# Performance work log

Hardware: AMD Instinct MI355X
Metric: run time of the kernel (lower is better)

The kernel has to match this reference:

```python
import jax, jax.numpy as jnp
import numpy as np

B, T, F_IN, NF, K, H, NOUT = 512, 800, 3, 128, 15, 150, 10
EPS = 1e-5


def hard_sigmoid(x):
    # Keras-style hard sigmoid used by LSTMHardSigmoid gates
    return jnp.clip(0.2 * x + 0.5, 0.0, 1.0)


def adabn(x, gamma, beta, axes):
    # AdaBN: normalize with current-batch statistics, then learned affine.
    m = jnp.mean(x, axis=axes, keepdims=True)
    v = jnp.var(x, axis=axes, keepdims=True)
    shape = [1] * x.ndim
    shape[1] = x.shape[1]
    return (x - m) * jax.lax.rsqrt(v + EPS) * gamma.reshape(shape) + beta.reshape(shape)


def lstm_dir(x_tbf, w_ih, w_hh, b_ih, b_hh):
    # x_tbf: (T', B, F). PyTorch gate order i, f, g, o; hard-sigmoid gates.
    pre = jnp.einsum('tbf,gf->tbg', x_tbf, w_ih) + b_ih + b_hh  # (T', B, 4H)
    bsz = x_tbf.shape[1]
    h0 = jnp.zeros((bsz, H), x_tbf.dtype)
    c0 = jnp.zeros((bsz, H), x_tbf.dtype)

    def step(carry, pre_t):
        h, c = carry
        gates = pre_t + h @ w_hh.T
        i, f, g, o = jnp.split(gates, 4, axis=-1)
        i = hard_sigmoid(i)
        f = hard_sigmoid(f)
        o = hard_sigmoid(o)
        g = jnp.tanh(g)
        c = f * c + i * g
        h = o * jnp.tanh(c)
        return (h, c), h

    _, hs = jax.lax.scan(step, (h0, c0), pre)
    return hs  # (T', B, H)


def setup_inputs() -> dict:
    key = jax.random.key(0)
    ks = jax.random.split(key, 12)
    s = lambda i, shape, sc=0.05: jax.random.normal(ks[i], shape, jnp.float32) * sc
    G = 4 * H
    return {
        'x': jax.random.normal(ks[0], (B, F_IN, T), jnp.float32),
        'conv_w': s(1, (NF, F_IN, K)),
        'conv_b': jnp.zeros((NF,), jnp.float32),
        'bn1_g': jnp.ones((NF,), jnp.float32),
        'bn1_b': jnp.zeros((NF,), jnp.float32),
        'w_ih_f': s(2, (G, NF)), 'w_hh_f': s(3, (G, H)),
        'b_ih_f': jnp.zeros((G,), jnp.float32), 'b_hh_f': jnp.zeros((G,), jnp.float32),
        'w_ih_b': s(4, (G, NF)), 'w_hh_b': s(5, (G, H)),
        'b_ih_b': jnp.zeros((G,), jnp.float32), 'b_hh_b': jnp.zeros((G,), jnp.float32),
        'bn2_g': jnp.ones((2 * H,), jnp.float32), 'bn2_b': jnp.zeros((2 * H,), jnp.float32),
        'fc1_w': s(6, (50, 2 * H)), 'fc1_b': jnp.zeros((50,), jnp.float32),
        'bn3_g': jnp.ones((50,), jnp.float32), 'bn3_b': jnp.zeros((50,), jnp.float32),
        'fc2_w': s(7, (NOUT, 50)), 'fc2_b': jnp.zeros((NOUT,), jnp.float32),
    }


def reference(x, conv_w, conv_b, bn1_g, bn1_b,
              w_ih_f, w_hh_f, b_ih_f, b_hh_f,
              w_ih_b, w_hh_b, b_ih_b, b_hh_b,
              bn2_g, bn2_b, fc1_w, fc1_b, bn3_g, bn3_b, fc2_w, fc2_b):
    # net1: Conv1d(3->128, k=15) + ReLU + (Dropout=identity in eval) + MaxPool1d(2)
    y = jax.lax.conv_general_dilated(x, conv_w, (1,), 'VALID',
                                     dimension_numbers=('NCH', 'OIH', 'NCH'))
    y = jax.nn.relu(y + conv_b[None, :, None])  # (B, 128, 786)
    L = y.shape[2] // 2
    y = y[:, :, :2 * L].reshape(y.shape[0], NF, L, 2).max(-1)  # (B, 128, 393)
    # net1_adabn (per-channel over batch and time)
    y = adabn(y, bn1_g, bn1_b, axes=(0, 2))
    # net2: bidirectional hard-sigmoid LSTM, batch_first; zero initial states
    seq = jnp.transpose(y, (2, 0, 1))  # (393, B, 128)
    h_f = lstm_dir(seq, w_ih_f, w_hh_f, b_ih_f, b_hh_f)
    h_b = lstm_dir(seq[::-1], w_ih_b, w_hh_b, b_ih_b, b_hh_b)[::-1]
    h = jnp.concatenate([h_f, h_b], axis=-1)  # (393, B, 300)
    # global max-pool over time (F.max_pool1d with kernel = full length)
    pooled = h.max(axis=0)  # (B, 300)
    z = adabn(pooled, bn2_g, bn2_b, axes=(0,))
    z = jax.nn.relu(z @ fc1_w.T + fc1_b)  # (B, 50)
    z = adabn(z, bn3_g, bn3_b, axes=(0,))
    logits = z @ fc2_w.T + fc2_b  # (B, 10)
    return jax.nn.softmax(logits, axis=1)
```

## Files before the change

### kernel.cpp

```cpp
#include <hip/hip_runtime.h>
#include <math.h>

#define B_   512
#define T_   800
#define FIN  3
#define NF   128
#define KW   15
#define HID  150
#define LOUT 393
#define G4   600
#define NPAD 640
#define EPS  1e-5f

#define NT_  38
#define KT_  5
#define HSTR 152
#define PNT  40
#define PKT  4
#define PSTR 648

typedef _Float16 half8 __attribute__((ext_vector_type(8)));
typedef _Float16 half4 __attribute__((ext_vector_type(4)));
typedef float f32x4 __attribute__((ext_vector_type(4)));

__device__ __forceinline__ float hsig(float x){ return fminf(fmaxf(0.2f*x+0.5f,0.f),1.f); }
__device__ __forceinline__ float ftanh(float x){ float e=__expf(2.f*x); return 1.f - 2.f/(e+1.f); }

__global__ __launch_bounds__(512) void k_conv2(const float* __restrict__ x,
        const float* __restrict__ cw, const float* __restrict__ cb,
        _Float16* __restrict__ y16, float* __restrict__ st){
  __shared__ float xs[FIN][800];
  __shared__ float wl[NF*FIN*KW];
  __shared__ float rs[4][128], rq[4][128];
  int tid = threadIdx.x;
  int b = blockIdx.x;
  for (int i=tid;i<FIN*800;i+=512) (&xs[0][0])[i] = x[(size_t)b*(FIN*T_) + i];
  for (int i=tid;i<NF*FIN*KW;i+=512) wl[i]=cw[i];
  __syncthreads();
  int c = tid & 127, li = tid >> 7;
  float wr[FIN*KW];
  #pragma unroll
  for (int i=0;i<FIN*KW;i++) wr[i]=wl[c*FIN*KW+i];
  float cbv = cb[c];
  float s=0.f, q=0.f;
  for (int l=li; l<LOUT; l+=4){
    float a0=0.f, a1=0.f;
    #pragma unroll
    for (int f=0;f<FIN;f++){
      const float2* xp = (const float2*)&xs[f][0] + l;
      float xv[16];
      #pragma unroll
      for (int p=0;p<8;p++){ float2 v=xp[p]; xv[2*p]=v.x; xv[2*p+1]=v.y; }
      #pragma unroll
      for (int k=0;k<KW;k++){ float w=wr[f*KW+k]; a0 += w*xv[k]; a1 += w*xv[k+1]; }
    }
    float v = fmaxf(fmaxf(a0,a1)+cbv, 0.f);
    y16[((size_t)b*LOUT + l)*NF + c] = (_Float16)v;
    s += v; q += v*v;
  }
  rs[li][c]=s; rq[li][c]=q;
  __syncthreads();
  if (tid < 128){
    float ts = rs[0][c]+rs[1][c]+rs[2][c]+rs[3][c];
    float tq = rq[0][c]+rq[1][c]+rq[2][c]+rq[3][c];
    atomicAdd(&st[c], ts);
    atomicAdd(&st[128+c], tq);
  }
}

__global__ void k_prep_bias(const float* __restrict__ st,
    const float* __restrict__ g1, const float* __restrict__ b1v,
    const float* __restrict__ wf, const float* __restrict__ wb,
    const float* __restrict__ bif, const float* __restrict__ bhf,
    const float* __restrict__ bib, const float* __restrict__ bhb,
    float* __restrict__ bef, float* __restrict__ beb){
  int id = blockIdx.x*256 + threadIdx.x;
  if (id >= 2*NPAD) return;
  int dir = id/NPAD, g = id%NPAD;
  float* be = dir? beb : bef;
  if (g >= G4){ be[g]=0.f; return; }
  int src = (g&3)*HID + (g>>2);
  const float* wih = dir? wb : wf;
  float bias = dir? (bib[src]+bhb[src]) : (bif[src]+bhf[src]);
  const float Ninv = 1.f/((float)B_*(float)LOUT);
  for (int f=0;f<NF;f++){
    float m = st[f]*Ninv;
    float var = st[NF+f]*Ninv - m*m;
    float a = g1[f]*rsqrtf(var+EPS);
    float d = b1v[f] - m*a;
    bias += d*wih[(size_t)src*NF+f];
  }
  be[g] = bias;
}

__global__ void k_prep_wih(const float* __restrict__ st,
    const float* __restrict__ g1,
    const float* __restrict__ wf, const float* __restrict__ wb,
    _Float16* __restrict__ wT16){
  int id = blockIdx.x*256 + threadIdx.x;
  if (id >= 2*PNT*PKT*64) return;
  int lane = id & 63;
  int kt = (id>>6) & 3;
  int nt = (id>>8) % PNT;
  int dir = id / (PNT*PKT*64);
  const float* wih = dir? wb : wf;
  int n = nt*16 + (lane&15);
  int src = (n&3)*HID + (n>>2);
  int kb = kt*32 + (lane>>4)*8;
  const float Ninv = 1.f/((float)B_*(float)LOUT);
  half8 v;
  #pragma unroll
  for (int j=0;j<8;j++){
    int k = kb+j;
    float m = st[k]*Ninv;
    float var = st[NF+k]*Ninv - m*m;
    float a = g1[k]*rsqrtf(var+EPS);
    float f = (n < G4) ? wih[(size_t)src*NF + k]*a : 0.f;
    v[j] = (_Float16)f;
  }
  *(half8*)&wT16[(size_t)id*8] = v;
}

__global__ void k_prep_whh(const float* __restrict__ whf, const float* __restrict__ whb,
                           _Float16* __restrict__ wfrag){
  int id = blockIdx.x*256 + threadIdx.x;
  if (id >= 2*NT_*KT_*64) return;
  int lane = id & 63;
  int rest = id >> 6;
  int kt = rest % KT_;
  int nt = (rest/KT_) % NT_;
  int dir = rest / (KT_*NT_);
  const float* wh = dir? whb : whf;
  int n = nt*16 + (lane&15);
  int src = (n&3)*HID + (n>>2);
  int kb = kt*32 + (lane>>4)*8;
  half8 v;
  #pragma unroll
  for (int j=0;j<8;j++){
    int k = kb + j;
    float f = (n < G4 && k < HID) ? wh[(size_t)src*HID + k] : 0.f;
    v[j] = (_Float16)f;
  }
  *(half8*)&wfrag[(size_t)id*8] = v;
}

__global__ __launch_bounds__(256) void k_proj2(const _Float16* __restrict__ y16,
    const _Float16* __restrict__ wT16,
    const float* __restrict__ bef, const float* __restrict__ beb,
    _Float16* __restrict__ pre16f, _Float16* __restrict__ pre16b,
    int t0f, int tc){
  __shared__ _Float16 Ds[128*136];
  __shared__ float bs[128];
  int dir = blockIdx.z;
  const _Float16* wfp = wT16 + (size_t)dir*PNT*PKT*64*8;
  const float* be = dir? beb : bef;
  _Float16* pre = dir? pre16b : pre16f;
  int tid = threadIdx.x, lane = tid&63, w = tid>>6;
  int trel = blockIdx.x>>2, bb = (blockIdx.x&3)*128;
  int t = dir ? (LOUT-1-t0f-trel) : (t0f+trel);
  int n0 = blockIdx.y*128;
  if (tid < 32) *(float4*)&bs[tid*4] = *(const float4*)&be[n0 + tid*4];

  f32x4 acc[2][8];
  #pragma unroll
  for (int i=0;i<2;i++)
    #pragma unroll
    for (int j=0;j<8;j++) acc[i][j] = (f32x4){0,0,0,0};

  int arow = lane&15, aq = (lane>>4)*8;
  const _Float16* a0p = y16 + ((size_t)(bb + (2*w)*16 + arow)*LOUT + t)*NF + aq;
  const _Float16* a1p = a0p + (size_t)16*LOUT*NF;
  int nb = n0 >> 4;
  #pragma unroll
  for (int kt=0; kt<PKT; kt++){
    half8 a0 = *(const half8*)(a0p + kt*32);
    half8 a1 = *(const half8*)(a1p + kt*32);
    #pragma unroll
    for (int nt=0; nt<8; nt++){
      half8 bf = *(const half8*)&wfp[(size_t)(((nb+nt)*PKT + kt)*64 + lane)*8];
      acc[0][nt] = __builtin_amdgcn_mfma_f32_16x16x32_f16(a0, bf, acc[0][nt], 0,0,0);
      acc[1][nt] = __builtin_amdgcn_mfma_f32_16x16x32_f16(a1, bf, acc[1][nt], 0,0,0);
    }
  }
  __syncthreads();
  int dcol = lane&15, dq = (lane>>4)*4;
  #pragma unroll
  for (int mi=0; mi<2; mi++){
    int rowb = (2*w+mi)*16 + dq;
    #pragma unroll
    for (int nt=0; nt<8; nt++){
      int colL = nt*16 + dcol;
      float bv = bs[colL];
      #pragma unroll
      for (int r=0;r<4;r++)
        Ds[(rowb+r)*136 + colL] = (_Float16)(acc[mi][nt][r] + bv);
    }
  }
  __syncthreads();
  int row = tid>>1, h = tid&1;
  const _Float16* src = &Ds[row*136 + h*64];
  _Float16* dst = pre + ((size_t)(trel*B_ + bb + row))*NPAD + n0 + h*64;
  #pragma unroll
  for (int qq=0; qq<8; qq++)
    *(float4*)(dst + qq*8) = *(const float4*)(src + qq*8);
}

__global__ __launch_bounds__(1024)
void k_rec5(const _Float16* __restrict__ wfrag,
            const _Float16* __restrict__ pref, const _Float16* __restrict__ preb,
            float* __restrict__ hst, float* __restrict__ cst, float* __restrict__ mst,
            float* __restrict__ pooled, int tc, int first, int last){
  int dir = blockIdx.x >> 5;
  int b0 = (blockIdx.x & 31) * 16;
  const _Float16* pre = dir? preb : pref;
  int tid = threadIdx.x;
  int lane = tid & 63, w = tid >> 6;

  __shared__ __align__(16) _Float16 hh[2][16][168];
  __shared__ __align__(16) _Float16 pls[2][16][PSTR];

  int cnt  = (w<6) ? 3 : 2;
  int base = (w<6) ? 3*w : 18 + 2*(w-6);
  const _Float16* wf = wfrag + (size_t)dir*NT_*KT_*64*8;
  half8 bfr[3][5];
  #pragma unroll
  for (int i=0;i<3;i++){
    #pragma unroll
    for (int kt=0;kt<KT_;kt++){
      int ntc = (i<cnt)? (base+i) : base;
      bfr[i][kt] = *(const half8*)&wf[(size_t)((ntc*KT_+kt)*64 + lane)*8];
    }
  }

  int batch = lane & 15;
  int uo[3]; bool uv[3];
  #pragma unroll
  for (int i=0;i<3;i++){
    uo[i] = (base+i)*4 + (lane>>4);
    uv[i] = (i<cnt) && (uo[i] < HID);
  }

  int srow0 = tid/80,        scol0 = (tid%80)*8;
  int srow1 = (tid+1024)/80, scol1 = ((tid+1024)%80)*8;
  bool s2 = tid < 256;

  for (int i=tid; i<2*16*168; i+=1024) (&hh[0][0][0])[i] = (_Float16)0.f;
  float c[3], m[3], hl[3];
  #pragma unroll
  for (int i=0;i<3;i++){ c[i]=0.f; m[i]=-1e30f; hl[i]=0.f; }
  __syncthreads();
  if (!first){
    #pragma unroll
    for (int i=0;i<3;i++){
      if (uv[i]){
        size_t gi = ((size_t)(dir*B_ + b0 + batch))*HSTR + uo[i];
        c[i]=cst[gi]; m[i]=mst[gi]; hl[i]=hst[gi];
        hh[0][batch][uo[i]] = (_Float16)hl[i];
      }
    }
  }
  {
    half8 s0 = *(const half8*)(pre + ((size_t)(b0 + srow0))*NPAD + scol0);
    *(half8*)&pls[0][srow0][scol0] = s0;
    if (s2){
      half8 s1 = *(const half8*)(pre + ((size_t)(b0 + srow1))*NPAD + scol1);
      *(half8*)&pls[0][srow1][scol1] = s1;
    }
  }
  __syncthreads();

  int cur = 0;
  for (int t=0; t<tc; t++){
    int nxt = cur ^ 1;
    half8 s0, s1;
    bool ld = (t+1 < tc);
    if (ld){
      size_t rbase = (size_t)(t+1)*B_ + b0;
      s0 = *(const half8*)(pre + (rbase + srow0)*NPAD + scol0);
      if (s2) s1 = *(const half8*)(pre + (rbase + srow1)*NPAD + scol1);
    }
    f32x4 acc0={0,0,0,0}, acc1={0,0,0,0}, acc2={0,0,0,0};
    #pragma unroll
    for (int kt=0; kt<KT_; kt++){
      half8 a = *(const half8*)&hh[cur][batch][kt*32 + (lane>>4)*8];
      acc0 = __builtin_amdgcn_mfma_f32_16x16x32_f16(bfr[0][kt], a, acc0, 0,0,0);
      acc1 = __builtin_amdgcn_mfma_f32_16x16x32_f16(bfr[1][kt], a, acc1, 0,0,0);
      if (cnt>2) acc2 = __builtin_amdgcn_mfma_f32_16x16x32_f16(bfr[2][kt], a, acc2, 0,0,0);
    }
    #define CELL(ACC, I)                                                     \
    if (uv[I]){                                                              \
      half4 pv = *(const half4*)&pls[cur][batch][4*uo[I]];                   \
      float xi = ACC[0] + (float)pv[0];                                      \
      float xf = ACC[1] + (float)pv[1];                                      \
      float xg = ACC[2] + (float)pv[2];                                      \
      float xo = ACC[3] + (float)pv[3];                                      \
      float ig=hsig(xi), fg=hsig(xf), og=hsig(xo), gg=ftanh(xg);             \
      c[I] = fg*c[I] + ig*gg;                                                \
      float hv = og*ftanh(c[I]);                                             \
      m[I] = fmaxf(m[I], hv);                                                \
      hl[I] = hv;                                                            \
      hh[nxt][batch][uo[I]] = (_Float16)hv;                                  \
    }
    CELL(acc0, 0)
    CELL(acc1, 1)
    CELL(acc2, 2)
    #undef CELL
    if (ld){
      *(half8*)&pls[nxt][srow0][scol0] = s0;
      if (s2) *(half8*)&pls[nxt][srow1][scol1] = s1;
    }
    __syncthreads();
    cur = nxt;
  }

  #pragma unroll
  for (int i=0;i<3;i++){
    if (uv[i]){
      size_t gi = ((size_t)(dir*B_ + b0 + batch))*HSTR + uo[i];
      cst[gi]=c[i]; mst[gi]=m[i]; hst[gi]=hl[i];
      if (last) pooled[(size_t)(b0+batch)*300 + dir*HID + uo[i]] = m[i];
    }
  }
}

__global__ void k_stats2(const float* __restrict__ pooled,
    const float* __restrict__ g2, const float* __restrict__ b2,
    float* __restrict__ a2, float* __restrict__ d2){
  int f = threadIdx.x;
  if (f >= 300) return;
  float s=0.f,q=0.f;
  for (int b=0;b<B_;b++){ float v = pooled[(size_t)b*300+f]; s+=v; q+=v*v; }
  float m = s*(1.f/B_), var = q*(1.f/B_) - m*m;
  float a = g2[f]*rsqrtf(var+EPS);
  a2[f]=a; d2[f]=b2[f]-m*a;
}

__global__ void k_fc1(const float* __restrict__ pooled,
    const float* __restrict__ a2, const float* __restrict__ d2,
    const float* __restrict__ w1, const float* __restrict__ fb1,
    float* __restrict__ z1){
  int o = blockIdx.x*256 + threadIdx.x;
  if (o >= B_*50) return;
  int b = o/50, j = o%50;
  float acc = fb1[j];
  for (int f=0;f<300;f++)
    acc += (a2[f]*pooled[(size_t)b*300+f] + d2[f]) * w1[j*300+f];
  z1[o] = fmaxf(acc,0.f);
}

__global__ void k_stats3(const float* __restrict__ z1,
    const float* __restrict__ g3, const float* __restrict__ b3,
    float* __restrict__ a3, float* __restrict__ d3){
  int f = threadIdx.x;
  if (f >= 50) return;
  float s=0.f,q=0.f;
  for (int b=0;b<B_;b++){ float v = z1[(size_t)b*50+f]; s+=v; q+=v*v; }
  float m = s*(1.f/B_), var = q*(1.f/B_) - m*m;
  float a = g3[f]*rsqrtf(var+EPS);
  a3[f]=a; d3[f]=b3[f]-m*a;
}

__global__ void k_fc2(const float* __restrict__ z1,
    const float* __restrict__ a3, const float* __restrict__ d3,
    const float* __restrict__ w2, const float* __restrict__ fb2,
    float* __restrict__ out){
  int b = blockIdx.x;
  int t = threadIdx.x;
  __shared__ float zl[50];
  __shared__ float lg[10];
  if (t<50) zl[t] = a3[t]*z1[(size_t)b*50+t] + d3[t];
  __syncthreads();
  if (t<10){
    float acc = fb2[t];
    for (int j=0;j<50;j++) acc += zl[j]*w2[t*50+j];
    lg[t]=acc;
  }
  __syncthreads();
  if (t<10){
    float m = lg[0];
    #pragma unroll
    for (int i=1;i<10;i++) m = fmaxf(m,lg[i]);
    float s = 0.f;
    #pragma unroll
    for (int i=0;i<10;i++) s += expf(lg[i]-m);
    out[(size_t)b*10+t] = expf(lg[t]-m)/s;
  }
}

extern "C" void kernel_launch(void* const* d_in, const int* in_sizes, int n_in,
                              void* d_out, int out_size, void* d_ws, size_t ws_size,
                              hipStream_t stream) {
  const float* x    = (const float*)d_in[0];
  const float* cw   = (const float*)d_in[1];
  const float* cb   = (const float*)d_in[2];
  const float* g1   = (const float*)d_in[3];
  const float* b1v  = (const float*)d_in[4];
  const float* wihf = (const float*)d_in[5];
  const float* whhf = (const float*)d_in[6];
  const float* bihf = (const float*)d_in[7];
  const float* bhhf = (const float*)d_in[8];
  const float* wihb = (const float*)d_in[9];
  const float* whhb = (const float*)d_in[10];
  const float* bihb = (const float*)d_in[11];
  const float* bhhb = (const float*)d_in[12];
  const float* g2   = (const float*)d_in[13];
  const float* b2   = (const float*)d_in[14];
  const float* w1   = (const float*)d_in[15];
  const float* fb1  = (const float*)d_in[16];
  const float* g3   = (const float*)d_in[17];
  const float* b3   = (const float*)d_in[18];
  const float* w2   = (const float*)d_in[19];
  const float* fb2  = (const float*)d_in[20];
  float* out = (float*)d_out;

  uint8_t* base = (uint8_t*)d_ws;
  size_t off = 0;
  auto allocB = [&](size_t nbytes)->uint8_t*{
    uint8_t* p = base + off;
    off = (off + nbytes + 255) & ~(size_t)255;
    return p;
  };
  _Float16* y16   = (_Float16*)allocB((size_t)B_*LOUT*NF*2);
  float* st       = (float*)allocB(256*4);
  _Float16* wT16  = (_Float16*)allocB((size_t)2*PNT*PKT*64*8*2);
  float* bef      = (float*)allocB(NPAD*4);
  float* beb      = (float*)allocB(NPAD*4);
  _Float16* wfrag = (_Float16*)allocB((size_t)2*NT_*KT_*64*8*2);
  float* hst      = (float*)allocB((size_t)2*B_*HSTR*4);
  float* cst      = (float*)allocB((size_t)2*B_*HSTR*4);
  float* mst      = (float*)allocB((size_t)2*B_*HSTR*4);
  float* pooled   = (float*)allocB((size_t)B_*300*4);
  float* a2       = (float*)allocB(320*4);
  float* d2       = (float*)allocB(320*4);
  float* z1       = (float*)allocB((size_t)B_*50*4);
  float* a3       = (float*)allocB(64*4);
  float* d3       = (float*)allocB(64*4);
  size_t fixedEnd = off;

  size_t per_t = (size_t)2*B_*NPAD*2;
  size_t avail = (ws_size > fixedEnd + 4096) ? (ws_size - fixedEnd - 4096) : 0;
  int tcmax = (int)(avail / per_t);
  if (tcmax < 1) tcmax = 1;
  if (tcmax > LOUT) tcmax = LOUT;
  int nch = (LOUT + tcmax - 1) / tcmax;
  int TC = (LOUT + nch - 1) / nch;
  _Float16* pre16f = (_Float16*)allocB((size_t)TC*B_*NPAD*2);
  _Float16* pre16b = (_Float16*)allocB((size_t)TC*B_*NPAD*2);

  hipMemsetAsync(st, 0, 256*4, stream);
  k_conv2<<<B_, 512, 0, stream>>>(x, cw, cb, y16, st);
  k_prep_bias<<<(2*NPAD+255)/256, 256, 0, stream>>>(st, g1, b1v, wihf, wihb,
                                                    bihf, bhhf, bihb, bhhb, bef, beb);
  k_prep_wih<<<(2*PNT*PKT*64+255)/256, 256, 0, stream>>>(st, g1, wihf, wihb, wT16);
  k_prep_whh<<<(2*NT_*KT_*64+255)/256, 256, 0, stream>>>(whhf, whhb, wfrag);

  int t0 = 0; int first = 1;
  while (t0 < LOUT){
    int tc = (TC < LOUT - t0) ? TC : (LOUT - t0);
    int lastc = (t0 + tc >= LOUT) ? 1 : 0;
    k_proj2<<<dim3(tc*4, 5, 2), 256, 0, stream>>>(y16, wT16, bef, beb,
                                                  pre16f, pre16b, t0, tc);
    k_rec5<<<64, 1024, 0, stream>>>(wfrag, pre16f, pre16b,
                                    hst, cst, mst, pooled, tc, first, lastc);
    t0 += tc; first = 0;
  }
  k_stats2<<<1, 320, 0, stream>>>(pooled, g2, b2, a2, d2);
  k_fc1<<<(B_*50+255)/256, 256, 0, stream>>>(pooled, a2, d2, w1, fb1, z1);
  k_stats3<<<1, 64, 0, stream>>>(z1, g3, b3, a3, d3);
  k_fc2<<<B_, 64, 0, stream>>>(z1, a3, d3, w2, fb2, out);
}
```

Before: 1.104 ms.

## Merge projection and recurrence into one kernel to overlap chunks

Folds the input-projection GEMM and the LSTM recurrence into a single kernel launch. The first 64 blocks run the recurrence on the current time chunk while the remaining blocks compute the projection for the next chunk into a double buffer, so idle CUs work during the serial recurrence. When the workspace can hold the whole sequence, it uses a single chunk, and the projection then becomes a separate launch followed by the recurrence. The projection blocks now run 1024 threads and write straight to global memory without LDS staging, which may hurt coalescing, and the large recurrence blocks limit co-residency.

```diff
diff --git a/kernel.cpp b/kernel.cpp
--- a/kernel.cpp
+++ b/kernel.cpp
@@ -144,181 +144,170 @@
   *(half8*)&wfrag[(size_t)id*8] = v;
 }
 
-__global__ __launch_bounds__(256) void k_proj2(const _Float16* __restrict__ y16,
-    const _Float16* __restrict__ wT16,
-    const float* __restrict__ bef, const float* __restrict__ beb,
-    _Float16* __restrict__ pre16f, _Float16* __restrict__ pre16b,
-    int t0f, int tc){
-  __shared__ _Float16 Ds[128*136];
-  __shared__ float bs[128];
-  int dir = blockIdx.z;
-  const _Float16* wfp = wT16 + (size_t)dir*PNT*PKT*64*8;
-  const float* be = dir? beb : bef;
-  _Float16* pre = dir? pre16b : pre16f;
-  int tid = threadIdx.x, lane = tid&63, w = tid>>6;
-  int trel = blockIdx.x>>2, bb = (blockIdx.x&3)*128;
-  int t = dir ? (LOUT-1-t0f-trel) : (t0f+trel);
-  int n0 = blockIdx.y*128;
-  if (tid < 32) *(float4*)&bs[tid*4] = *(const float4*)&be[n0 + tid*4];
-
-  f32x4 acc[2][8];
-  #pragma unroll
-  for (int i=0;i<2;i++)
-    #pragma unroll
-    for (int j=0;j<8;j++) acc[i][j] = (f32x4){0,0,0,0};
-
-  int arow = lane&15, aq = (lane>>4)*8;
-  const _Float16* a0p = y16 + ((size_t)(bb + (2*w)*16 + arow)*LOUT + t)*NF + aq;
-  const _Float16* a1p = a0p + (size_t)16*LOUT*NF;
-  int nb = n0 >> 4;
-  #pragma unroll
-  for (int kt=0; kt<PKT; kt++){
-    half8 a0 = *(const half8*)(a0p + kt*32);
-    half8 a1 = *(const half8*)(a1p + kt*32);
-    #pragma unroll
-    for (int nt=0; nt<8; nt++){
-      half8 bf = *(const half8*)&wfp[(size_t)(((nb+nt)*PKT + kt)*64 + lane)*8];
-      acc[0][nt] = __builtin_amdgcn_mfma_f32_16x16x32_f16(a0, bf, acc[0][nt], 0,0,0);
-      acc[1][nt] = __builtin_amdgcn_mfma_f32_16x16x32_f16(a1, bf, acc[1][nt], 0,0,0);
-    }
-  }
-  __syncthreads();
-  int dcol = lane&15, dq = (lane>>4)*4;
-  #pragma unroll
-  for (int mi=0; mi<2; mi++){
-    int rowb = (2*w+mi)*16 + dq;
-    #pragma unroll
-    for (int nt=0; nt<8; nt++){
-      int colL = nt*16 + dcol;
-      float bv = bs[colL];
-      #pragma unroll
-      for (int r=0;r<4;r++)
-        Ds[(rowb+r)*136 + colL] = (_Float16)(acc[mi][nt][r] + bv);
-    }
-  }
-  __syncthreads();
-  int row = tid>>1, h = tid&1;
-  const _Float16* src = &Ds[row*136 + h*64];
-  _Float16* dst = pre + ((size_t)(trel*B_ + bb + row))*NPAD + n0 + h*64;
-  #pragma unroll
-  for (int qq=0; qq<8; qq++)
-    *(float4*)(dst + qq*8) = *(const float4*)(src + qq*8);
-}
-
 __global__ __launch_bounds__(1024)
-void k_rec5(const _Float16* __restrict__ wfrag,
-            const _Float16* __restrict__ pref, const _Float16* __restrict__ preb,
+void k_mega(const _Float16* __restrict__ wfrag,
+            const _Float16* __restrict__ wT16,
+            const float* __restrict__ bef, const float* __restrict__ beb,
+            const _Float16* __restrict__ y16,
+            const _Float16* __restrict__ prf, const _Float16* __restrict__ prb,
+            _Float16* __restrict__ pwf, _Float16* __restrict__ pwb,
             float* __restrict__ hst, float* __restrict__ cst, float* __restrict__ mst,
-            float* __restrict__ pooled, int tc, int first, int last){
-  int dir = blockIdx.x >> 5;
-  int b0 = (blockIdx.x & 31) * 16;
-  const _Float16* pre = dir? preb : pref;
-  int tid = threadIdx.x;
-  int lane = tid & 63, w = tid >> 6;
-
+            float* __restrict__ pooled,
+            int nrec, int tc, int first, int last, int t0p){
   __shared__ __align__(16) _Float16 hh[2][16][168];
   __shared__ __align__(16) _Float16 pls[2][16][PSTR];
-
-  int cnt  = (w<6) ? 3 : 2;
-  int base = (w<6) ? 3*w : 18 + 2*(w-6);
-  const _Float16* wf = wfrag + (size_t)dir*NT_*KT_*64*8;
-  half8 bfr[3][5];
-  #pragma unroll
-  for (int i=0;i<3;i++){
-    #pragma unroll
-    for (int kt=0;kt<KT_;kt++){
-      int ntc = (i<cnt)? (base+i) : base;
-      bfr[i][kt] = *(const half8*)&wf[(size_t)((ntc*KT_+kt)*64 + lane)*8];
-    }
-  }
-
-  int batch = lane & 15;
-  int uo[3]; bool uv[3];
-  #pragma unroll
-  for (int i=0;i<3;i++){
-    uo[i] = (base+i)*4 + (lane>>4);
-    uv[i] = (i<cnt) && (uo[i] < HID);
-  }
-
-  int srow0 = tid/80,        scol0 = (tid%80)*8;
-  int srow1 = (tid+1024)/80, scol1 = ((tid+1024)%80)*8;
-  bool s2 = tid < 256;
-
-  for (int i=tid; i<2*16*168; i+=1024) (&hh[0][0][0])[i] = (_Float16)0.f;
-  float c[3], m[3], hl[3];
-  #pragma unroll
-  for (int i=0;i<3;i++){ c[i]=0.f; m[i]=-1e30f; hl[i]=0.f; }
-  __syncthreads();
-  if (!first){
+  int tid = threadIdx.x;
+  int bid = blockIdx.x;
+
+  if (bid < nrec){
+    int dir = bid >> 5;
+    int b0 = (bid & 31) * 16;
+    const _Float16* pre = dir? prb : prf;
+    int lane = tid & 63, w = tid >> 6;
+
+    int cnt  = (w<6) ? 3 : 2;
+    int base = (w<6) ? 3*w : 18 + 2*(w-6);
+    const _Float16* wf = wfrag + (size_t)dir*NT_*KT_*64*8;
+    half8 bfr[3][5];
+    #pragma unroll
+    for (int i=0;i<3;i++){
+      #pragma unroll
+      for (int kt=0;kt<KT_;kt++){
+        int ntc = (i<cnt)? (base+i) : base;
+        bfr[i][kt] = *(const half8*)&wf[(size_t)((ntc*KT_+kt)*64 + lane)*8];
+      }
+    }
+
+    int batch = lane & 15;
+    int uo[3]; bool uv[3];
+    #pragma unroll
+    for (int i=0;i<3;i++){
+      uo[i] = (base+i)*4 + (lane>>4);
+      uv[i] = (i<cnt) && (uo[i] < HID);
+    }
+
+    int srow0 = tid/80,        scol0 = (tid%80)*8;
+    int srow1 = (tid+1024)/80, scol1 = ((tid+1024)%80)*8;
+    bool s2 = tid < 256;
+
+    for (int i=tid; i<2*16*168; i+=1024) (&hh[0][0][0])[i] = (_Float16)0.f;
+    float c[3], m[3], hl[3];
+    #pragma unroll
+    for (int i=0;i<3;i++){ c[i]=0.f; m[i]=-1e30f; hl[i]=0.f; }
+    __syncthreads();
+    if (!first){
+      #pragma unroll
+      for (int i=0;i<3;i++){
+        if (uv[i]){
+          size_t gi = ((size_t)(dir*B_ + b0 + batch))*HSTR + uo[i];
+          c[i]=cst[gi]; m[i]=mst[gi]; hl[i]=hst[gi];
+          hh[0][batch][uo[i]] = (_Float16)hl[i];
+        }
+      }
+    }
+    {
+      half8 s0 = *(const half8*)(pre + ((size_t)(b0 + srow0))*NPAD + scol0);
+      *(half8*)&pls[0][srow0][scol0] = s0;
+      if (s2){
+        half8 s1 = *(const half8*)(pre + ((size_t)(b0 + srow1))*NPAD + scol1);
+        *(half8*)&pls[0][srow1][scol1] = s1;
+      }
+    }
+    __syncthreads();
+
+    int cur = 0;
+    for (int t=0; t<tc; t++){
+      int nxt = cur ^ 1;
+      half8 s0, s1;
+      bool ld = (t+1 < tc);
+      if (ld){
+        size_t rbase = (size_t)(t+1)*B_ + b0;
+        s0 = *(const half8*)(pre + (rbase + srow0)*NPAD + scol0);
+        if (s2) s1 = *(const half8*)(pre + (rbase + srow1)*NPAD + scol1);
+      }
+      f32x4 acc0={0,0,0,0}, acc1={0,0,0,0}, acc2={0,0,0,0};
+      #pragma unroll
+      for (int kt=0; kt<KT_; kt++){
+        half8 a = *(const half8*)&hh[cur][batch][kt*32 + (lane>>4)*8];
+        acc0 = __builtin_amdgcn_mfma_f32_16x16x32_f16(bfr[0][kt], a, acc0, 0,0,0);
+        acc1 = __builtin_amdgcn_mfma_f32_16x16x32_f16(bfr[1][kt], a, acc1, 0,0,0);
+        if (cnt>2) acc2 = __builtin_amdgcn_mfma_f32_16x16x32_f16(bfr[2][kt], a, acc2, 0,0,0);
+      }
+      #define CELL(ACC, I)                                                     \
+      if (uv[I]){                                                              \
+        half4 pv = *(const half4*)&pls[cur][batch][4*uo[I]];                   \
+        float xi = ACC[0] + (float)pv[0];                                      \
+        float xf = ACC[1] + (float)pv[1];                                      \
+        float xg = ACC[2] + (float)pv[2];                                      \
+        float xo = ACC[3] + (float)pv[3];                                      \
+        float ig=hsig(xi), fg=hsig(xf), og=hsig(xo), gg=ftanh(xg);             \
+        c[I] = fg*c[I] + ig*gg;                                                \
+        float hv = og*ftanh(c[I]);                                             \
+        m[I] = fmaxf(m[I], hv);                                                \
+        hl[I] = hv;                                                            \
+        hh[nxt][batch][uo[I]] = (_Float16)hv;                                  \
+      }
+      CELL(acc0, 0)
+      CELL(acc1, 1)
+      CELL(acc2, 2)
+      #undef CELL
+      if (ld){
+        *(half8*)&pls[nxt][srow0][scol0] = s0;
+        if (s2) *(half8*)&pls[nxt][srow1][scol1] = s1;
+      }
+      __syncthreads();
+      cur = nxt;
+    }
+
     #pragma unroll
     for (int i=0;i<3;i++){
       if (uv[i]){
         size_t gi = ((size_t)(dir*B_ + b0 + batch))*HSTR + uo[i];
-        c[i]=cst[gi]; m[i]=mst[gi]; hl[i]=hst[gi];
-        hh[0][batch][uo[i]] = (_Float16)hl[i];
-      }
-    }
-  }
+        cst[gi]=c[i]; mst[gi]=m[i]; hst[gi]=hl[i];
+        if (last) pooled[(size_t)(b0+batch)*300 + dir*HID + uo[i]] = m[i];
+      }
+    }
+    return;
+  }
+
   {
-    half8 s0 = *(const half8*)(pre + ((size_t)(b0 + srow0))*NPAD + scol0);
-    *(half8*)&pls[0][srow0][scol0] = s0;
-    if (s2){
-      half8 s1 = *(const half8*)(pre + ((size_t)(b0 + srow1))*NPAD + scol1);
-      *(half8*)&pls[0][srow1][scol1] = s1;
-    }
-  }
-  __syncthreads();
-
-  int cur = 0;
-  for (int t=0; t<tc; t++){
-    int nxt = cur ^ 1;
-    half8 s0, s1;
-    bool ld = (t+1 < tc);
-    if (ld){
-      size_t rbase = (size_t)(t+1)*B_ + b0;
-      s0 = *(const half8*)(pre + (rbase + srow0)*NPAD + scol0);
-      if (s2) s1 = *(const half8*)(pre + (rbase + srow1)*NPAD + scol1);
-    }
-    f32x4 acc0={0,0,0,0}, acc1={0,0,0,0}, acc2={0,0,0,0};
-    #pragma unroll
-    for (int kt=0; kt<KT_; kt++){
-      half8 a = *(const half8*)&hh[cur][batch][kt*32 + (lane>>4)*8];
-      acc0 = __builtin_amdgcn_mfma_f32_16x16x32_f16(bfr[0][kt], a, acc0, 0,0,0);
-      acc1 = __builtin_amdgcn_mfma_f32_16x16x32_f16(bfr[1][kt], a, acc1, 0,0,0);
-      if (cnt>2) acc2 = __builtin_amdgcn_mfma_f32_16x16x32_f16(bfr[2][kt], a, acc2, 0,0,0);
-    }
-    #define CELL(ACC, I)                                                     \
-    if (uv[I]){                                                              \
-      half4 pv = *(const half4*)&pls[cur][batch][4*uo[I]];                   \
-      float xi = ACC[0] + (float)pv[0];                                      \
-      float xf = ACC[1] + (float)pv[1];                                      \
-      float xg = ACC[2] + (float)pv[2];                                      \
-      float xo = ACC[3] + (float)pv[3];                                      \
-      float ig=hsig(xi), fg=hsig(xf), og=hsig(xo), gg=ftanh(xg);             \
-      c[I] = fg*c[I] + ig*gg;                                                \
-      float hv = og*ftanh(c[I]);                                             \
-      m[I] = fmaxf(m[I], hv);                                                \
-      hl[I] = hv;                                                            \
-      hh[nxt][batch][uo[I]] = (_Float16)hv;                                  \
-    }
-    CELL(acc0, 0)
-    CELL(acc1, 1)
-    CELL(acc2, 2)
-    #undef CELL
-    if (ld){
-      *(half8*)&pls[nxt][srow0][scol0] = s0;
-      if (s2) *(half8*)&pls[nxt][srow1][scol1] = s1;
-    }
-    __syncthreads();
-    cur = nxt;
-  }
-
-  #pragma unroll
-  for (int i=0;i<3;i++){
-    if (uv[i]){
-      size_t gi = ((size_t)(dir*B_ + b0 + batch))*HSTR + uo[i];
-      cst[gi]=c[i]; mst[gi]=m[i]; hst[gi]=hl[i];
-      if (last) pooled[(size_t)(b0+batch)*300 + dir*HID + uo[i]] = m[i];
+    int pb = bid - nrec;
+    int dir  = pb & 1;
+    int t5   = pb >> 1;
+    int by   = t5 % 5;
+    int t2   = t5 / 5;
+    int mb   = t2 & 1;
+    int trel = t2 >> 1;
+    const _Float16* wfp = wT16 + (size_t)dir*PNT*PKT*64*8;
+    const float* be = dir? beb : bef;
+    _Float16* pre = dir? pwb : pwf;
+    int t = dir ? (LOUT-1-t0p-trel) : (t0p+trel);
+    int n0 = by*128, nb = n0>>4;
+    int lane = tid & 63, ww = tid >> 6;
+    int m0 = mb*256 + ww*16;
+    int arow = lane&15, aq = (lane>>4)*8;
+    const _Float16* ap = y16 + ((size_t)(m0+arow)*LOUT + t)*NF + aq;
+    f32x4 acc[8];
+    #pragma unroll
+    for (int j=0;j<8;j++) acc[j] = (f32x4){0,0,0,0};
+    #pragma unroll
+    for (int kt=0; kt<PKT; kt++){
+      half8 a = *(const half8*)(ap + kt*32);
+      #pragma unroll
+      for (int nt=0; nt<8; nt++){
+        half8 bf = *(const half8*)&wfp[(size_t)(((nb+nt)*PKT + kt)*64 + lane)*8];
+        acc[nt] = __builtin_amdgcn_mfma_f32_16x16x32_f16(a, bf, acc[nt], 0,0,0);
+      }
+    }
+    int dcol = lane&15, dq = (lane>>4)*4;
+    size_t rowg = (size_t)trel*B_ + m0 + dq;
+    #pragma unroll
+    for (int nt=0; nt<8; nt++){
+      int colL = n0 + nt*16 + dcol;
+      float bv = be[colL];
+      #pragma unroll
+      for (int r=0;r<4;r++)
+        pre[(rowg+r)*NPAD + colL] = (_Float16)(acc[nt][r] + bv);
     }
   }
 }
@@ -437,15 +426,29 @@
   float* d3       = (float*)allocB(64*4);
   size_t fixedEnd = off;
 
-  size_t per_t = (size_t)2*B_*NPAD*2;
   size_t avail = (ws_size > fixedEnd + 4096) ? (ws_size - fixedEnd - 4096) : 0;
-  int tcmax = (int)(avail / per_t);
-  if (tcmax < 1) tcmax = 1;
-  if (tcmax > LOUT) tcmax = LOUT;
-  int nch = (LOUT + tcmax - 1) / tcmax;
-  int TC = (LOUT + nch - 1) / nch;
-  _Float16* pre16f = (_Float16*)allocB((size_t)TC*B_*NPAD*2);
-  _Float16* pre16b = (_Float16*)allocB((size_t)TC*B_*NPAD*2);
+  size_t per_t1 = (size_t)2*B_*NPAD*2;
+  size_t per_t2 = (size_t)4*B_*NPAD*2;
+  int nch, TC;
+  if (avail / per_t1 >= (size_t)LOUT){
+    nch = 1; TC = LOUT;
+  } else {
+    int tcmax = (int)(avail / per_t2);
+    if (tcmax < 1) tcmax = 1;
+    if (tcmax > LOUT) tcmax = LOUT;
+    nch = (LOUT + tcmax - 1) / tcmax;
+    TC = (LOUT + nch - 1) / nch;
+  }
+  _Float16* preA_f = (_Float16*)allocB((size_t)TC*B_*NPAD*2);
+  _Float16* preA_b = (_Float16*)allocB((size_t)TC*B_*NPAD*2);
+  _Float16* preB_f = preA_f;
+  _Float16* preB_b = preA_b;
+  if (nch > 1){
+    preB_f = (_Float16*)allocB((size_t)TC*B_*NPAD*2);
+    preB_b = (_Float16*)allocB((size_t)TC*B_*NPAD*2);
+  }
+  auto t0of = [&](int k){ return k*TC; };
+  auto tcof = [&](int k){ int r = LOUT - k*TC; return (r < TC) ? r : TC; };
 
   hipMemsetAsync(st, 0, 256*4, stream);
   k_conv2<<<B_, 512, 0, stream>>>(x, cw, cb, y16, st);
@@ -454,16 +457,21 @@
   k_prep_wih<<<(2*PNT*PKT*64+255)/256, 256, 0, stream>>>(st, g1, wihf, wihb, wT16);
   k_prep_whh<<<(2*NT_*KT_*64+255)/256, 256, 0, stream>>>(whhf, whhb, wfrag);
 
-  int t0 = 0; int first = 1;
-  while (t0 < LOUT){
-    int tc = (TC < LOUT - t0) ? TC : (LOUT - t0);
-    int lastc = (t0 + tc >= LOUT) ? 1 : 0;
-    k_proj2<<<dim3(tc*4, 5, 2), 256, 0, stream>>>(y16, wT16, bef, beb,
-                                                  pre16f, pre16b, t0, tc);
-    k_rec5<<<64, 1024, 0, stream>>>(wfrag, pre16f, pre16b,
-                                    hst, cst, mst, pooled, tc, first, lastc);
-    t0 += tc; first = 0;
-  }
+  k_mega<<<tcof(0)*20, 1024, 0, stream>>>(wfrag, wT16, bef, beb, y16,
+      preA_f, preA_b, preA_f, preA_b, hst, cst, mst, pooled,
+      0, 0, 0, 0, t0of(0));
+  for (int k=0; k<nch; k++){
+    int hasN = (k+1 < nch) ? 1 : 0;
+    _Float16* rf = (k & 1) ? preB_f : preA_f;
+    _Float16* rb = (k & 1) ? preB_b : preA_b;
+    _Float16* wf_ = ((k+1) & 1) ? preB_f : preA_f;
+    _Float16* wb_ = ((k+1) & 1) ? preB_b : preA_b;
+    int grid = 64 + (hasN ? tcof(k+1)*20 : 0);
+    k_mega<<<grid, 1024, 0, stream>>>(wfrag, wT16, bef, beb, y16,
+        rf, rb, wf_, wb_, hst, cst, mst, pooled,
+        64, tcof(k), (k==0) ? 1 : 0, hasN ? 0 : 1, hasN ? t0of(k+1) : 0);
+  }
+
   k_stats2<<<1, 320, 0, stream>>>(pooled, g2, b2, a2, d2);
   k_fc1<<<(B_*50+255)/256, 256, 0, stream>>>(pooled, a2, d2, w1, fb1, z1);
   k_stats3<<<1, 64, 0, stream>>>(z1, g3, b3, a3, d3);
```

Result: faster. 895.1 us (-18.9%).
